# Kernel tuning notes

Measured on AMD Instinct MI355X. Metric: run time of the kernel, lower is better.

Reference implementation:

```python
import jax, jax.numpy as jnp
import numpy as np
from jax import lax

EPS = 1e-8

def setup_inputs() -> dict:
    key = jax.random.key(0)
    k1, k2, k3, k4 = jax.random.split(key, 4)
    b, ic, oc, ks, sd, h, w = 16, 512, 512, 3, 512, 64, 64
    x = jax.random.normal(k1, (b, ic, h, w), dtype=jnp.float32)
    style = jax.random.normal(k2, (b, sd), dtype=jnp.float32)
    # kaiming_normal_(fan_in, linear): std = 1/sqrt(ic*ks*ks)
    weight = jax.random.normal(k3, (oc, ic, ks, ks), dtype=jnp.float32) / np.sqrt(ic * ks * ks)
    bias = jnp.zeros((oc,), dtype=jnp.float32)
    # nn.Linear default init ~ U(-1/sqrt(sd), 1/sqrt(sd)); normal approx is fine for a baseline
    mod_w = jax.random.normal(k4, (ic, sd), dtype=jnp.float32) / np.sqrt(sd)
    mod_b = jnp.ones((ic,), dtype=jnp.float32)  # bias initialized to 1.0 in the module
    return {"x": x, "style": style, "weight": weight, "bias": bias, "mod_w": mod_w, "mod_b": mod_b}

def reference(x, style, weight, bias, mod_w, mod_b):
    b, ic, h, w = x.shape
    oc, _, ks, _ = weight.shape
    # style modulation: [b, ic]
    s = style @ mod_w.T + mod_b
    # per-sample modulated weights: [b, oc, ic, k, k]
    wmod = weight[None] * s[:, None, :, None, None]
    # demodulation
    demod = lax.rsqrt(jnp.sum(wmod * wmod, axis=(2, 3, 4)) + EPS)  # [b, oc]
    wmod = wmod * demod[:, :, None, None, None]
    pad = ks // 2
    # grouped conv with groups=b == per-sample conv: vmap over batch
    def conv1(xi, wi):  # xi: [ic,h,w], wi: [oc,ic,k,k]
        return lax.conv_general_dilated(
            xi[None], wi, window_strides=(1, 1),
            padding=[(pad, pad), (pad, pad)],
            dimension_numbers=("NCHW", "OIHW", "NCHW"))[0]
    out = jax.vmap(conv1)(x, wmod)  # [b, oc, h, w]
    return out + bias[None, :, None, None]
```

## Files before the change

kernel.cpp:

```cpp
#include <hip/hip_runtime.h>
#include <hip/hip_bf16.h>


typedef __bf16 bf16x8 __attribute__((ext_vector_type(8)));
typedef float  f32x4  __attribute__((ext_vector_type(4)));

#define IC   512
#define OC   512
#define HW   4096
#define KTOT 4608

typedef __attribute__((address_space(3))) unsigned lds_u32;
typedef const __attribute__((address_space(1))) unsigned glb_u32;
#define GLL16(gsrc, ldst) \
    __builtin_amdgcn_global_load_lds((glb_u32*)(gsrc), (lds_u32*)(ldst), 16, 0, 0)
#define BAR()   asm volatile("s_barrier" ::: "memory")

template<int N> __device__ __forceinline__ void vmw() {
    asm volatile("s_waitcnt vmcnt(%0)" :: "n"(N) : "memory");
}

#define MFMA1(A, B, C) __builtin_amdgcn_mfma_f32_16x16x32_bf16(A, B, C, 0, 0, 0)

__global__ __launch_bounds__(256) void style_mod_kernel(
    const float* __restrict__ style, const float* __restrict__ mod_w,
    const float* __restrict__ mod_b, float* __restrict__ s_out)
{
    int pair = blockIdx.x * 4 + (threadIdx.x >> 6);
    int lane = threadIdx.x & 63;
    int b = pair >> 9;
    int i = pair & 511;
    const float4* sv = (const float4*)(style + b * 512);
    const float4* wv = (const float4*)(mod_w + i * 512);
    float4 a0 = sv[lane * 2], a1 = sv[lane * 2 + 1];
    float4 w0 = wv[lane * 2], w1 = wv[lane * 2 + 1];
    float sum = a0.x*w0.x + a0.y*w0.y + a0.z*w0.z + a0.w*w0.w
              + a1.x*w1.x + a1.y*w1.y + a1.z*w1.z + a1.w*w1.w;
    #pragma unroll
    for (int off = 32; off; off >>= 1) sum += __shfl_xor(sum, off);
    if (lane == 0) s_out[pair] = sum + mod_b[i];
}

__global__ __launch_bounds__(256) void wmod_kernel(
    const float* __restrict__ weight,
    const float* __restrict__ s_in,
    __hip_bfloat16* __restrict__ wmod)
{
    int oc = blockIdx.x;
    __shared__ float w_sh[4608];
    __shared__ float s_sh[8192];
    __shared__ float q_sh[512];
    __shared__ float demod_sh[16];
    int t = threadIdx.x;
    const float* wrow = weight + (size_t)oc * KTOT;
    for (int e = t; e < 4608; e += 256) w_sh[e] = wrow[e];
    for (int e = t; e < 8192; e += 256) s_sh[e] = s_in[e];
    __syncthreads();
    for (int ic = t; ic < 512; ic += 256) {
        float q = 0.f;
        #pragma unroll
        for (int tap = 0; tap < 9; ++tap) { float w = w_sh[ic * 9 + tap]; q += w * w; }
        q_sh[ic] = q;
    }
    __syncthreads();
    int bb = t >> 4, li = t & 15;
    float part = 0.f;
    for (int ic = li; ic < 512; ic += 16) {
        float sv = s_sh[bb * 512 + ic];
        part += q_sh[ic] * sv * sv;
    }
    #pragma unroll
    for (int off = 8; off; off >>= 1) part += __shfl_xor(part, off, 16);
    if (li == 0) demod_sh[bb] = rsqrtf(part + 1e-8f);
    __syncthreads();
    for (int b2 = 0; b2 < 16; ++b2) {
        float dm = demod_sh[b2];
        const float* srow = s_sh + b2 * 512;
        __hip_bfloat16* dst = wmod + ((size_t)b2 * 512 + oc) * KTOT;
        for (int ep = t; ep < 4608; ep += 256) {
            int tap = ep >> 9, ic = ep & 511;
            dst[ep] = __float2bfloat16(w_sh[ic * 9 + tap] * srow[ic] * dm);
        }
    }
}

__global__ void zero_row_kernel(__hip_bfloat16* xT) {
    ((unsigned*)(xT + ((size_t)blockIdx.x * 4097 + 4096) * 512))[threadIdx.x] = 0u;
}

__global__ __launch_bounds__(256) void xpose_kernel(
    const float* __restrict__ x, __hip_bfloat16* __restrict__ xT)
{
    __shared__ __align__(16) float tile[64][68];
    int b = blockIdx.z, ic0 = blockIdx.y * 64, p0 = blockIdx.x * 64;
    int t = threadIdx.x;
    const float* xb = x + ((size_t)b * 512 + ic0) * 4096 + p0;
    int rr = t >> 4, cc = (t & 15) * 4;
    #pragma unroll
    for (int i = 0; i < 4; ++i) {
        float4 v = *(const float4*)(xb + (size_t)(rr + i * 16) * 4096 + cc);
        *(float4*)&tile[rr + i * 16][cc] = v;
    }
    __syncthreads();
    int pr = t >> 2, io = (t & 3) * 16;
    __hip_bfloat16 obuf[16];
    #pragma unroll
    for (int j = 0; j < 16; ++j) obuf[j] = __float2bfloat16(tile[io + j][pr]);
    __hip_bfloat16* dst = xT + ((size_t)b * 4097 + p0 + pr) * 512 + ic0 + io;
    *(uint4*)dst       = *(uint4*)&obuf[0];
    *(uint4*)(dst + 8) = *(uint4*)&obuf[8];
}

__global__ __launch_bounds__(512, 2) void conv_kernel(
    const __hip_bfloat16* __restrict__ xT,
    const __hip_bfloat16* __restrict__ wmod,
    const float* __restrict__ bias,
    float* __restrict__ out)
{
    __shared__ __align__(16) __hip_bfloat16 Ash[4][256 * 32];
    __shared__ __align__(16) __hip_bfloat16 Bsh[4][256 * 32];

    const int t    = threadIdx.x;
    const int lane = t & 63;
    const int wid  = t >> 6;
    const int wm   = wid >> 2;
    const int wn   = wid & 3;
    const int lr   = lane & 15;
    const int lq   = lane >> 4;

    int bid = blockIdx.x;
    int xcd = bid & 7, idx = bid >> 3;
    int oc1 = idx & 1;
    int nt  = (idx >> 1) & 15;
    int bb  = (idx >> 5) & 1;
    int b   = xcd * 2 + bb;
    int oc0 = oc1 * 256, n0 = nt * 256;

    const __hip_bfloat16* wb = wmod + (size_t)(b * 512 + oc0) * KTOT;
    const __hip_bfloat16* xb = xT + (size_t)b * 4097 * 512;

    const int qoff = (((t & 3) ^ ((t >> 3) & 3)) * 8);
    const int srow = t >> 2;
    const int p0g  = n0 + srow;
    const int y0p  = p0g >> 6, x0p = p0g & 63;

    const __hip_bfloat16* pA0 = wb + (size_t)srow * KTOT + qoff;
    const __hip_bfloat16* pA1 = pA0 + (size_t)128 * KTOT;

    const int swq = (lq ^ ((lr >> 1) & 3)) * 8;
    const int arb = (wm * 128 + lr) * 32 + swq;
    const int brb = (wn * 64  + lr) * 32 + swq;

    f32x4 acc[8][4] = {};
    bf16x8 aL[2][4], bR[2][4];

    auto bptrs = [&](int tap, const __hip_bfloat16*& P0, const __hip_bfloat16*& P1) {
        int dy = tap / 3 - 1, dx = tap % 3 - 1;
        int sy = y0p + dy, sx = x0p + dx;
        int pix0 = ((((unsigned)sy)  < 64u) & (((unsigned)sx) < 64u)) ? ((sy  << 6) + sx) : 4096;
        int sy1 = sy + 2;
        int pix1 = ((((unsigned)sy1) < 64u) & (((unsigned)sx) < 64u)) ? ((sy1 << 6) + sx) : 4096;
        P0 = xb + (size_t)pix0 * 512 + qoff;
        P1 = xb + (size_t)pix1 * 512 + qoff;
    };

#define STAGE_A(SB, OFF) { \
    GLL16(pA0 + (OFF), &Ash[SB][t * 8]); \
    GLL16(pA1 + (OFF), &Ash[SB][(t + 512) * 8]); }
#define STAGE_B(SB, Q0, Q1, OFF) { \
    GLL16((Q0) + (OFF), &Bsh[SB][t * 8]); \
    GLL16((Q1) + (OFF), &Bsh[SB][(t + 512) * 8]); }

#define STEP(CH, DO_STAGE, DO_PF, NQ0, NQ1, VN, DO_VMW) { \
    const int cs = (CH) & 3, ps = ((CH) + 1) & 3, ss = ((CH) + 3) & 3; \
    const int cp = (CH) & 1, np = ((CH) + 1) & 1; \
    bf16x8 ah0 = *(const bf16x8*)(&Ash[cs][arb + 2048]); \
    bf16x8 ah1 = *(const bf16x8*)(&Ash[cs][arb + 2560]); \
    bf16x8 ah2 = *(const bf16x8*)(&Ash[cs][arb + 3072]); \
    bf16x8 ah3 = *(const bf16x8*)(&Ash[cs][arb + 3584]); \
    if (DO_STAGE) { \
        STAGE_A(ss, ((CH) + 3) * 32); \
        if ((CH) < 13) { STAGE_B(ss, pB0, pB1, ((CH) + 3) * 32); } \
        else           { STAGE_B(ss, NQ0, NQ1, ((CH) - 13) * 32); } \
    } \
    __builtin_amdgcn_s_setprio(1); \
    _Pragma("unroll") for (int ni = 0; ni < 4; ++ni) { \
        acc[0][ni] = MFMA1(aL[cp][0], bR[cp][ni], acc[0][ni]); \
        acc[1][ni] = MFMA1(aL[cp][1], bR[cp][ni], acc[1][ni]); \
        acc[2][ni] = MFMA1(aL[cp][2], bR[cp][ni], acc[2][ni]); \
        acc[3][ni] = MFMA1(aL[cp][3], bR[cp][ni], acc[3][ni]); \
    } \
    __builtin_amdgcn_s_setprio(0); \
    if (DO_PF) { \
        _Pragma("unroll") for (int mi = 0; mi < 4; ++mi) \
            aL[np][mi] = *(const bf16x8*)(&Ash[ps][arb + mi * 512]); \
        _Pragma("unroll") for (int ni = 0; ni < 4; ++ni) \
            bR[np][ni] = *(const bf16x8*)(&Bsh[ps][brb + ni * 512]); \
    } \
    __builtin_amdgcn_s_setprio(1); \
    _Pragma("unroll") for (int ni = 0; ni < 4; ++ni) { \
        acc[4][ni] = MFMA1(ah0, bR[cp][ni], acc[4][ni]); \
        acc[5][ni] = MFMA1(ah1, bR[cp][ni], acc[5][ni]); \
        acc[6][ni] = MFMA1(ah2, bR[cp][ni], acc[6][ni]); \
        acc[7][ni] = MFMA1(ah3, bR[cp][ni], acc[7][ni]); \
    } \
    __builtin_amdgcn_s_setprio(0); \
    if (DO_VMW) { vmw<VN>(); } \
    BAR(); }

    const __hip_bfloat16 *pB0, *pB1, *nB0, *nB1;
    bptrs(0, pB0, pB1);

    STAGE_A(0, 0);  STAGE_B(0, pB0, pB1, 0);
    STAGE_A(1, 32); STAGE_B(1, pB0, pB1, 32);
    STAGE_A(2, 64); STAGE_B(2, pB0, pB1, 64);
    vmw<4>();
    BAR();
    #pragma unroll
    for (int mi = 0; mi < 4; ++mi)
        aL[0][mi] = *(const bf16x8*)(&Ash[0][arb + mi * 512]);
    #pragma unroll
    for (int ni = 0; ni < 4; ++ni)
        bR[0][ni] = *(const bf16x8*)(&Bsh[0][brb + ni * 512]);

    for (int tap = 0; tap < 8; ++tap) {
        bptrs(tap + 1, nB0, nB1);
        #pragma unroll
        for (int ch = 0; ch < 16; ++ch) {
            STEP(ch, true, true, nB0, nB1, 4, true);
        }
        pA0 += 512; pA1 += 512;
        pB0 = nB0; pB1 = nB1;
    }

    #pragma unroll
    for (int ch = 0; ch < 13; ++ch) {
        STEP(ch, true, true, nB0, nB1, 4, true);
    }
    STEP(13, false, true, nB0, nB1, 0, true);
    STEP(14, false, true, nB0, nB1, 0, false);
    {
        bf16x8 ah0 = *(const bf16x8*)(&Ash[3][arb + 2048]);
        bf16x8 ah1 = *(const bf16x8*)(&Ash[3][arb + 2560]);
        bf16x8 ah2 = *(const bf16x8*)(&Ash[3][arb + 3072]);
        bf16x8 ah3 = *(const bf16x8*)(&Ash[3][arb + 3584]);
        #pragma unroll
        for (int ni = 0; ni < 4; ++ni) {
            acc[0][ni] = MFMA1(aL[1][0], bR[1][ni], acc[0][ni]);
            acc[1][ni] = MFMA1(aL[1][1], bR[1][ni], acc[1][ni]);
            acc[2][ni] = MFMA1(aL[1][2], bR[1][ni], acc[2][ni]);
            acc[3][ni] = MFMA1(aL[1][3], bR[1][ni], acc[3][ni]);
            acc[4][ni] = MFMA1(ah0, bR[1][ni], acc[4][ni]);
            acc[5][ni] = MFMA1(ah1, bR[1][ni], acc[5][ni]);
            acc[6][ni] = MFMA1(ah2, bR[1][ni], acc[6][ni]);
            acc[7][ni] = MFMA1(ah3, bR[1][ni], acc[7][ni]);
        }
    }
#undef STEP
#undef STAGE_A
#undef STAGE_B

    #pragma unroll
    for (int mi = 0; mi < 8; ++mi) {
        int oc = oc0 + wm * 128 + mi * 16 + lq * 4;
        #pragma unroll
        for (int ni = 0; ni < 4; ++ni) {
            int n = n0 + wn * 64 + ni * 16 + lr;
            #pragma unroll
            for (int v = 0; v < 4; ++v) {
                float r = acc[mi][ni][v] + bias[oc + v];
                out[((size_t)(b * OC + oc + v)) * HW + n] = r;
            }
        }
    }
}

extern "C" void kernel_launch(void* const* d_in, const int* in_sizes, int n_in,
                              void* d_out, int out_size, void* d_ws, size_t ws_size,
                              hipStream_t stream) {
    const float* x      = (const float*)d_in[0];
    const float* style  = (const float*)d_in[1];
    const float* weight = (const float*)d_in[2];
    const float* bias   = (const float*)d_in[3];
    const float* mod_w  = (const float*)d_in[4];
    const float* mod_b  = (const float*)d_in[5];
    float* out = (float*)d_out;

    float* s_ws = (float*)d_ws;
    __hip_bfloat16* wmod = (__hip_bfloat16*)((char*)d_ws + 32768);
    __hip_bfloat16* xT   = (__hip_bfloat16*)((char*)d_ws + 32768 + (size_t)16 * 512 * KTOT * 2);

    style_mod_kernel<<<2048, 256, 0, stream>>>(style, mod_w, mod_b, s_ws);
    wmod_kernel<<<512, 256, 0, stream>>>(weight, s_ws, wmod);
    zero_row_kernel<<<16, 256, 0, stream>>>(xT);
    dim3 tgrid(64, 8, 16);
    xpose_kernel<<<tgrid, 256, 0, stream>>>(x, xT);
    conv_kernel<<<512, 512, 0, stream>>>(xT, wmod, bias, out);
}
```

Baseline: 358.8 us.

## Use 4 waves with 128x128 warp tiles in conv kernel

Cuts the conv block from 8 waves to 4, so each wave computes a 128x128 output tile (8x8 MFMA accumulators) instead of 128x64. Each thread now issues four global-to-LDS loads per operand per stage, and the software pipeline is simplified to one fragment prefetch followed by one MFMA batch. The goal is more register-level reuse of A/B fragments and fewer LDS reads per MFMA. In exchange it needs 256 accumulator registers per thread, runs only one 4-wave block per CU, and has less latency hiding, with a real risk of register spills.

```diff
diff --git a/kernel.cpp b/kernel.cpp
--- a/kernel.cpp
+++ b/kernel.cpp
@@ -111,7 +111,7 @@
     *(uint4*)(dst + 8) = *(uint4*)&obuf[8];
 }
 
-__global__ __launch_bounds__(512, 2) void conv_kernel(
+__global__ __launch_bounds__(256, 1) void conv_kernel(
     const __hip_bfloat16* __restrict__ xT,
     const __hip_bfloat16* __restrict__ wmod,
     const float* __restrict__ bias,
@@ -123,8 +123,8 @@
     const int t    = threadIdx.x;
     const int lane = t & 63;
     const int wid  = t >> 6;
-    const int wm   = wid >> 2;
-    const int wn   = wid & 3;
+    const int wm   = wid >> 1;
+    const int wn   = wid & 1;
     const int lr   = lane & 15;
     const int lq   = lane >> 4;
 
@@ -145,118 +145,100 @@
     const int y0p  = p0g >> 6, x0p = p0g & 63;
 
     const __hip_bfloat16* pA0 = wb + (size_t)srow * KTOT + qoff;
-    const __hip_bfloat16* pA1 = pA0 + (size_t)128 * KTOT;
+    const __hip_bfloat16* pA1 = pA0 + (size_t)64  * KTOT;
+    const __hip_bfloat16* pA2 = pA0 + (size_t)128 * KTOT;
+    const __hip_bfloat16* pA3 = pA0 + (size_t)192 * KTOT;
 
     const int swq = (lq ^ ((lr >> 1) & 3)) * 8;
     const int arb = (wm * 128 + lr) * 32 + swq;
-    const int brb = (wn * 64  + lr) * 32 + swq;
-
-    f32x4 acc[8][4] = {};
-    bf16x8 aL[2][4], bR[2][4];
-
-    auto bptrs = [&](int tap, const __hip_bfloat16*& P0, const __hip_bfloat16*& P1) {
+    const int brb = (wn * 128 + lr) * 32 + swq;
+
+    f32x4 acc[8][8] = {};
+    bf16x8 fA[2][8], fB[2][8];
+
+    const __hip_bfloat16 *pB0, *pB1, *pB2, *pB3, *nB0, *nB1, *nB2, *nB3;
+    auto bptrs = [&](int tap, const __hip_bfloat16*& P0, const __hip_bfloat16*& P1,
+                     const __hip_bfloat16*& P2, const __hip_bfloat16*& P3) {
         int dy = tap / 3 - 1, dx = tap % 3 - 1;
-        int sy = y0p + dy, sx = x0p + dx;
-        int pix0 = ((((unsigned)sy)  < 64u) & (((unsigned)sx) < 64u)) ? ((sy  << 6) + sx) : 4096;
-        int sy1 = sy + 2;
-        int pix1 = ((((unsigned)sy1) < 64u) & (((unsigned)sx) < 64u)) ? ((sy1 << 6) + sx) : 4096;
-        P0 = xb + (size_t)pix0 * 512 + qoff;
-        P1 = xb + (size_t)pix1 * 512 + qoff;
+        int sx = x0p + dx;
+        bool okx = ((unsigned)sx < 64u);
+        int sy0 = y0p + dy;
+        int q0 = (okx & ((unsigned)(sy0    ) < 64u)) ? ((sy0    ) * 64 + sx) : 4096;
+        int q1 = (okx & ((unsigned)(sy0 + 1) < 64u)) ? ((sy0 + 1) * 64 + sx) : 4096;
+        int q2 = (okx & ((unsigned)(sy0 + 2) < 64u)) ? ((sy0 + 2) * 64 + sx) : 4096;
+        int q3 = (okx & ((unsigned)(sy0 + 3) < 64u)) ? ((sy0 + 3) * 64 + sx) : 4096;
+        P0 = xb + (size_t)q0 * 512 + qoff;
+        P1 = xb + (size_t)q1 * 512 + qoff;
+        P2 = xb + (size_t)q2 * 512 + qoff;
+        P3 = xb + (size_t)q3 * 512 + qoff;
     };
 
 #define STAGE_A(SB, OFF) { \
     GLL16(pA0 + (OFF), &Ash[SB][t * 8]); \
-    GLL16(pA1 + (OFF), &Ash[SB][(t + 512) * 8]); }
-#define STAGE_B(SB, Q0, Q1, OFF) { \
+    GLL16(pA1 + (OFF), &Ash[SB][(t + 256) * 8]); \
+    GLL16(pA2 + (OFF), &Ash[SB][(t + 512) * 8]); \
+    GLL16(pA3 + (OFF), &Ash[SB][(t + 768) * 8]); }
+#define STAGE_B(SB, Q0, Q1, Q2, Q3, OFF) { \
     GLL16((Q0) + (OFF), &Bsh[SB][t * 8]); \
-    GLL16((Q1) + (OFF), &Bsh[SB][(t + 512) * 8]); }
-
-#define STEP(CH, DO_STAGE, DO_PF, NQ0, NQ1, VN, DO_VMW) { \
-    const int cs = (CH) & 3, ps = ((CH) + 1) & 3, ss = ((CH) + 3) & 3; \
+    GLL16((Q1) + (OFF), &Bsh[SB][(t + 256) * 8]); \
+    GLL16((Q2) + (OFF), &Bsh[SB][(t + 512) * 8]); \
+    GLL16((Q3) + (OFF), &Bsh[SB][(t + 768) * 8]); }
+
+#define PF(P, SL) { \
+    _Pragma("unroll") for (int mi = 0; mi < 8; ++mi) \
+        fA[P][mi] = *(const bf16x8*)(&Ash[SL][arb + mi * 512]); \
+    _Pragma("unroll") for (int ni = 0; ni < 8; ++ni) \
+        fB[P][ni] = *(const bf16x8*)(&Bsh[SL][brb + ni * 512]); }
+
+#define MM(P) { \
+    __builtin_amdgcn_s_setprio(1); \
+    _Pragma("unroll") for (int mi = 0; mi < 8; ++mi) \
+        _Pragma("unroll") for (int ni = 0; ni < 8; ++ni) \
+            acc[mi][ni] = MFMA1(fA[P][mi], fB[P][ni], acc[mi][ni]); \
+    __builtin_amdgcn_s_setprio(0); }
+
+#define STEP(CH, DO_STAGE, BNXT) { \
+    const int sl = ((CH) + 1) & 3, ss = ((CH) + 3) & 3; \
     const int cp = (CH) & 1, np = ((CH) + 1) & 1; \
-    bf16x8 ah0 = *(const bf16x8*)(&Ash[cs][arb + 2048]); \
-    bf16x8 ah1 = *(const bf16x8*)(&Ash[cs][arb + 2560]); \
-    bf16x8 ah2 = *(const bf16x8*)(&Ash[cs][arb + 3072]); \
-    bf16x8 ah3 = *(const bf16x8*)(&Ash[cs][arb + 3584]); \
     if (DO_STAGE) { \
         STAGE_A(ss, ((CH) + 3) * 32); \
-        if ((CH) < 13) { STAGE_B(ss, pB0, pB1, ((CH) + 3) * 32); } \
-        else           { STAGE_B(ss, NQ0, NQ1, ((CH) - 13) * 32); } \
+        if ((CH) < 13) { STAGE_B(ss, pB0, pB1, pB2, pB3, ((CH) + 3) * 32); } \
+        else           { STAGE_B(ss, BNXT##0, BNXT##1, BNXT##2, BNXT##3, ((CH) - 13) * 32); } \
     } \
-    __builtin_amdgcn_s_setprio(1); \
-    _Pragma("unroll") for (int ni = 0; ni < 4; ++ni) { \
-        acc[0][ni] = MFMA1(aL[cp][0], bR[cp][ni], acc[0][ni]); \
-        acc[1][ni] = MFMA1(aL[cp][1], bR[cp][ni], acc[1][ni]); \
-        acc[2][ni] = MFMA1(aL[cp][2], bR[cp][ni], acc[2][ni]); \
-        acc[3][ni] = MFMA1(aL[cp][3], bR[cp][ni], acc[3][ni]); \
-    } \
-    __builtin_amdgcn_s_setprio(0); \
-    if (DO_PF) { \
-        _Pragma("unroll") for (int mi = 0; mi < 4; ++mi) \
-            aL[np][mi] = *(const bf16x8*)(&Ash[ps][arb + mi * 512]); \
-        _Pragma("unroll") for (int ni = 0; ni < 4; ++ni) \
-            bR[np][ni] = *(const bf16x8*)(&Bsh[ps][brb + ni * 512]); \
-    } \
-    __builtin_amdgcn_s_setprio(1); \
-    _Pragma("unroll") for (int ni = 0; ni < 4; ++ni) { \
-        acc[4][ni] = MFMA1(ah0, bR[cp][ni], acc[4][ni]); \
-        acc[5][ni] = MFMA1(ah1, bR[cp][ni], acc[5][ni]); \
-        acc[6][ni] = MFMA1(ah2, bR[cp][ni], acc[6][ni]); \
-        acc[7][ni] = MFMA1(ah3, bR[cp][ni], acc[7][ni]); \
-    } \
-    __builtin_amdgcn_s_setprio(0); \
-    if (DO_VMW) { vmw<VN>(); } \
+    PF(np, sl); \
+    MM(cp); \
+    vmw<8>(); \
     BAR(); }
 
-    const __hip_bfloat16 *pB0, *pB1, *nB0, *nB1;
-    bptrs(0, pB0, pB1);
-
-    STAGE_A(0, 0);  STAGE_B(0, pB0, pB1, 0);
-    STAGE_A(1, 32); STAGE_B(1, pB0, pB1, 32);
-    STAGE_A(2, 64); STAGE_B(2, pB0, pB1, 64);
-    vmw<4>();
+    bptrs(0, pB0, pB1, pB2, pB3);
+
+    STAGE_A(0, 0);  STAGE_B(0, pB0, pB1, pB2, pB3, 0);
+    STAGE_A(1, 32); STAGE_B(1, pB0, pB1, pB2, pB3, 32);
+    STAGE_A(2, 64); STAGE_B(2, pB0, pB1, pB2, pB3, 64);
+    vmw<16>();
     BAR();
-    #pragma unroll
-    for (int mi = 0; mi < 4; ++mi)
-        aL[0][mi] = *(const bf16x8*)(&Ash[0][arb + mi * 512]);
-    #pragma unroll
-    for (int ni = 0; ni < 4; ++ni)
-        bR[0][ni] = *(const bf16x8*)(&Bsh[0][brb + ni * 512]);
+    PF(0, 0);
 
     for (int tap = 0; tap < 8; ++tap) {
-        bptrs(tap + 1, nB0, nB1);
+        bptrs(tap + 1, nB0, nB1, nB2, nB3);
         #pragma unroll
         for (int ch = 0; ch < 16; ++ch) {
-            STEP(ch, true, true, nB0, nB1, 4, true);
+            STEP(ch, true, nB);
         }
-        pA0 += 512; pA1 += 512;
-        pB0 = nB0; pB1 = nB1;
+        pA0 += 512; pA1 += 512; pA2 += 512; pA3 += 512;
+        pB0 = nB0; pB1 = nB1; pB2 = nB2; pB3 = nB3;
     }
 
     #pragma unroll
     for (int ch = 0; ch < 13; ++ch) {
-        STEP(ch, true, true, nB0, nB1, 4, true);
-    }
-    STEP(13, false, true, nB0, nB1, 0, true);
-    STEP(14, false, true, nB0, nB1, 0, false);
-    {
-        bf16x8 ah0 = *(const bf16x8*)(&Ash[3][arb + 2048]);
-        bf16x8 ah1 = *(const bf16x8*)(&Ash[3][arb + 2560]);
-        bf16x8 ah2 = *(const bf16x8*)(&Ash[3][arb + 3072]);
-        bf16x8 ah3 = *(const bf16x8*)(&Ash[3][arb + 3584]);
-        #pragma unroll
-        for (int ni = 0; ni < 4; ++ni) {
-            acc[0][ni] = MFMA1(aL[1][0], bR[1][ni], acc[0][ni]);
-            acc[1][ni] = MFMA1(aL[1][1], bR[1][ni], acc[1][ni]);
-            acc[2][ni] = MFMA1(aL[1][2], bR[1][ni], acc[2][ni]);
-            acc[3][ni] = MFMA1(aL[1][3], bR[1][ni], acc[3][ni]);
-            acc[4][ni] = MFMA1(ah0, bR[1][ni], acc[4][ni]);
-            acc[5][ni] = MFMA1(ah1, bR[1][ni], acc[5][ni]);
-            acc[6][ni] = MFMA1(ah2, bR[1][ni], acc[6][ni]);
-            acc[7][ni] = MFMA1(ah3, bR[1][ni], acc[7][ni]);
-        }
-    }
+        STEP(ch, true, nB);
+    }
+    { PF(0, 2); MM(1); vmw<0>(); BAR(); }
+    { PF(1, 3); MM(0); }
+    MM(1);
 #undef STEP
+#undef PF
+#undef MM
 #undef STAGE_A
 #undef STAGE_B
 
@@ -264,8 +246,8 @@
     for (int mi = 0; mi < 8; ++mi) {
         int oc = oc0 + wm * 128 + mi * 16 + lq * 4;
         #pragma unroll
-        for (int ni = 0; ni < 4; ++ni) {
-            int n = n0 + wn * 64 + ni * 16 + lr;
+        for (int ni = 0; ni < 8; ++ni) {
+            int n = n0 + wn * 128 + ni * 16 + lr;
             #pragma unroll
             for (int v = 0; v < 4; ++v) {
                 float r = acc[mi][ni][v] + bias[oc + v];
@@ -295,5 +277,5 @@
     zero_row_kernel<<<16, 256, 0, stream>>>(xT);
     dim3 tgrid(64, 8, 16);
     xpose_kernel<<<tgrid, 256, 0, stream>>>(x, xT);
-    conv_kernel<<<512, 512, 0, stream>>>(xT, wmod, bias, out);
-}
+    conv_kernel<<<512, 256, 0, stream>>>(xT, wmod, bias, out);
+}
```

New measurement: 374.2 us. 1.04x slower.
